# Optimization experiments

Measured on AMD Instinct MI355X. Metric: run time of the kernel, lower is better.

## Reference

```python
import jax, jax.numpy as jnp
import numpy as np

N_HEAD, D_MODEL, D_K, D_V = 8, 512, 64, 64
B, S = 4, 2048
LN_EPS = 1e-5


def setup_inputs() -> dict:
    key = jax.random.key(0)
    ks = jax.random.split(key, 12)
    std_qk = np.sqrt(2.0 / (D_MODEL + D_K))
    std_v = np.sqrt(2.0 / (D_MODEL + D_V))
    return {
        "q": jax.random.normal(ks[0], (B, S, D_MODEL), jnp.float32),
        "k": jax.random.normal(ks[1], (B, S, D_MODEL), jnp.float32),
        "v": jax.random.normal(ks[2], (B, S, D_MODEL), jnp.float32),
        "w_qs": jax.random.normal(ks[3], (N_HEAD * D_K, D_MODEL), jnp.float32) * std_qk,
        "b_qs": jnp.zeros((N_HEAD * D_K,), jnp.float32),
        "w_ks": jax.random.normal(ks[4], (N_HEAD * D_K, D_MODEL), jnp.float32) * std_qk,
        "b_ks": jnp.zeros((N_HEAD * D_K,), jnp.float32),
        "w_vs": jax.random.normal(ks[5], (N_HEAD * D_V, D_MODEL), jnp.float32) * std_v,
        "b_vs": jnp.zeros((N_HEAD * D_V,), jnp.float32),
        "w_fc": jax.random.normal(ks[6], (D_MODEL, N_HEAD * D_V), jnp.float32) * np.sqrt(2.0 / (D_MODEL + N_HEAD * D_V)),
        "b_fc": jnp.zeros((D_MODEL,), jnp.float32),
        "ln_g": jnp.ones((D_MODEL,), jnp.float32),
        "ln_b": jnp.zeros((D_MODEL,), jnp.float32),
    }


def reference(q, k, v, w_qs, b_qs, w_ks, b_ks, w_vs, b_vs, w_fc, b_fc, ln_g, ln_b):
    sz_b, len_q, _ = q.shape
    residual = q
    temperature = np.power(D_K, 0.5).astype(np.float32)
    # Projections: [b, s, h*dk] -> [h, b, s, dk]  (matches permute(2,0,1,3))
    qh = (jnp.einsum('bsd,fd->bsf', q, w_qs) + b_qs).reshape(sz_b, len_q, N_HEAD, D_K).transpose(2, 0, 1, 3)
    kh = (jnp.einsum('bsd,fd->bsf', k, w_ks) + b_ks).reshape(sz_b, -1, N_HEAD, D_K).transpose(2, 0, 1, 3)
    vh = (jnp.einsum('bsd,fd->bsf', v, w_vs) + b_vs).reshape(sz_b, -1, N_HEAD, D_V).transpose(2, 0, 1, 3)
    # Scaled dot-product attention (dropout is identity in eval)
    attn = jnp.einsum('hbqd,hbkd->hbqk', qh, kh) / temperature
    attn = jax.nn.softmax(attn, axis=-1)
    out = jnp.einsum('hbqk,hbkv->hbqv', attn, vh)          # [h, b, q, dv]
    out = out.transpose(1, 2, 0, 3).reshape(sz_b, len_q, N_HEAD * D_V)
    out = jnp.einsum('bsf,df->bsd', out, w_fc) + b_fc
    # Residual + LayerNorm
    x = out + residual
    mu = jnp.mean(x, axis=-1, keepdims=True)
    var = jnp.mean(jnp.square(x - mu), axis=-1, keepdims=True)
    x = (x - mu) * jax.lax.rsqrt(var + LN_EPS) * ln_g + ln_b
    # attn returned as [(n_head*b), len_q, len_k] to match torch bmm layout
    return x, attn.reshape(N_HEAD * sz_b, len_q, -1)
```

## Files before the change

kernel.cpp:

```cpp
#include <hip/hip_runtime.h>
#include <hip/hip_bf16.h>

constexpr int NB  = 4;
constexpr int NS  = 2048;
constexpr int NH  = 8;
constexpr int DM  = 512;
constexpr int DKV = 64;
constexpr int HB  = NH * NB;

typedef __attribute__((ext_vector_type(8))) short short8;
typedef __attribute__((ext_vector_type(4))) float f32x4;

__device__ inline unsigned short f2bf(float f) {
    unsigned u = __builtin_bit_cast(unsigned, f);
    u = (u + 0x7fffu + ((u >> 16) & 1u)) >> 16;
    return (unsigned short)u;
}
__device__ inline float bf2f(unsigned short h) {
    unsigned u = ((unsigned)h) << 16;
    return __builtin_bit_cast(float, u);
}
__device__ inline short8 ld8(const unsigned short* p) { return *(const short8*)p; }

__device__ inline short8 pack8(const float* p) {
    f32x4 a = *(const f32x4*)p;
    f32x4 b = *(const f32x4*)(p + 4);
    short8 r;
    r[0] = (short)f2bf(a[0]); r[1] = (short)f2bf(a[1]);
    r[2] = (short)f2bf(a[2]); r[3] = (short)f2bf(a[3]);
    r[4] = (short)f2bf(b[0]); r[5] = (short)f2bf(b[1]);
    r[6] = (short)f2bf(b[2]); r[7] = (short)f2bf(b[3]);
    return r;
}

__device__ inline f32x4 mfma16(short8 a, short8 b, f32x4 c) {
    return __builtin_amdgcn_mfma_f32_16x16x32_bf16(a, b, c, 0, 0, 0);
}

__device__ inline void gl_lds16(const void* g, void* l) {
    __builtin_amdgcn_global_load_lds(
        (const __attribute__((address_space(1))) unsigned*)g,
        (__attribute__((address_space(3))) unsigned*)l, 16, 0, 0);
}

__device__ inline void bar() { __builtin_amdgcn_s_barrier(); }

__global__ __launch_bounds__(256) void k_cvtw(const float* __restrict__ s0,
                                              const float* __restrict__ s1,
                                              const float* __restrict__ s2,
                                              const float* __restrict__ s3,
                                              unsigned short* __restrict__ d0,
                                              unsigned short* __restrict__ d1,
                                              unsigned short* __restrict__ d2,
                                              unsigned short* __restrict__ d3)
{
    const float* s; unsigned short* d;
    switch (blockIdx.y) {
        case 0:  s = s0; d = d0; break;
        case 1:  s = s1; d = d1; break;
        case 2:  s = s2; d = d2; break;
        default: s = s3; d = d3; break;
    }
    const size_t i = ((size_t)blockIdx.x * 256 + threadIdx.x) * 8;
    *(short8*)(d + i) = pack8(s + i);
}

__global__ __launch_bounds__(256, 4) void k_proj3(const float* __restrict__ Xq,
                                                  const float* __restrict__ Xk,
                                                  const float* __restrict__ Xv,
                                                  const unsigned short* __restrict__ Wq,
                                                  const unsigned short* __restrict__ Wk,
                                                  const unsigned short* __restrict__ Wv,
                                                  const float* __restrict__ bq,
                                                  const float* __restrict__ bk,
                                                  const float* __restrict__ bv,
                                                  unsigned short* __restrict__ oq,
                                                  unsigned short* __restrict__ ok,
                                                  unsigned short* __restrict__ ov)
{
    const float* X; const unsigned short* W; const float* bias; unsigned short* out;
    float scale = 1.0f; int vtrans = 0;
    switch (blockIdx.z) {
        case 0:  X = Xq; W = Wq; bias = bq; out = oq;
                 scale = 0.125f * 1.44269504088896340736f; break;
        case 1:  X = Xk; W = Wk; bias = bk; out = ok; break;
        default: X = Xv; W = Wv; bias = bv; out = ov; vtrans = 1; break;
    }
    const int tid = threadIdx.x;
    const int l = tid & 63, w = tid >> 6;
    const int c = l & 15, g = l >> 4;
    const int m0 = blockIdx.y * 64 + w * 16;
    const int f0 = blockIdx.x * 64;
    const int arow = m0 + c;

    f32x4 acc[4] = {};
    const float* aB = X + (size_t)arow * DM;
    for (int kb = 0; kb < DM; kb += 32) {
        short8 af = pack8(aB + kb + g * 8);
#pragma unroll
        for (int n = 0; n < 4; ++n) {
            short8 bf = ld8(W + (size_t)(f0 + n * 16 + c) * DM + kb + g * 8);
            acc[n] = mfma16(af, bf, acc[n]);
        }
    }
#pragma unroll
    for (int n = 0; n < 4; ++n) {
        const int f = f0 + n * 16 + c;
        const int h = f >> 6, d = f & 63;
        const float bvv = bias[f];
#pragma unroll
        for (int r = 0; r < 4; ++r) {
            const int m = m0 + g * 4 + r;
            const int bb = m >> 11, s = m & (NS - 1);
            const int hb = h * NB + bb;
            const float v = (acc[n][r] + bvv) * scale;
            const size_t idx = vtrans ? ((size_t)(hb * DKV + d) * NS + s)
                                      : ((size_t)(hb * NS + s) * DKV + d);
            out[idx] = f2bf(v);
        }
    }
}

__global__ __launch_bounds__(256, 4) void k_attn(const unsigned short* __restrict__ Qh,
                                                 const unsigned short* __restrict__ Kh,
                                                 const unsigned short* __restrict__ Vt,
                                                 float* __restrict__ attn,
                                                 unsigned short* __restrict__ Obuf)
{
    __shared__ __align__(16) char kld[2][8192];
    __shared__ __align__(16) char vld[2][8192];
    __shared__ __align__(16) char plds[4 * 2048];
    const int tid = threadIdx.x;
    const int l = tid & 63, w = tid >> 6;
    const int c = l & 15, g = l >> 4;
    constexpr int NT = NS / 64;

    const int bid = blockIdx.x;
    const int wid = (bid & 7) * 128 + (bid >> 3);
    const int hb = wid >> 5;
    const int q0 = (wid & 31) * 64 + w * 16;
    char* myp = plds + w * 2048;

    const char* kbytes = (const char*)(Kh + (size_t)hb * NS * DKV);
    const char* vbytes = (const char*)(Vt + (size_t)hb * DKV * NS);

    const unsigned short* qb = Qh + ((size_t)hb * NS + q0 + c) * DKV + g * 8;
    const short8 qf0 = ld8(qb), qf1 = ld8(qb + 32);

    int koff[2], voff[2];
#pragma unroll
    for (int j = 0; j < 2; ++j) {
        const int D = (w * 2 + j) * 1024 + l * 16;
        const int row = D >> 7;
        const int scolb = (D & 127) ^ ((row & 7) << 4);
        koff[j] = row * 128 + scolb;
        voff[j] = row * (NS * 2) + scolb;
    }
    const int swc = (c & 7) << 4;

    const int ldsbase = w * 2048;

    float ls[4] = {0.f, 0.f, 0.f, 0.f};
    {
        gl_lds16(kbytes + koff[0], kld[0] + ldsbase);
        gl_lds16(kbytes + koff[1], kld[0] + ldsbase + 1024);
        asm volatile("s_waitcnt vmcnt(0)" ::: "memory");
        bar();
        __builtin_amdgcn_sched_barrier(0);
        int cur = 0;
        for (int kt = 0; kt < NT; ++kt) {
            if (kt + 1 < NT) {
                const size_t nb = (size_t)(kt + 1) * 64 * 128;
                gl_lds16(kbytes + nb + koff[0], kld[cur ^ 1] + ldsbase);
                gl_lds16(kbytes + nb + koff[1], kld[cur ^ 1] + ldsbase + 1024);
            }
            if (kt > 0) {
                if (kt + 1 < NT) { asm volatile("s_waitcnt vmcnt(2)" ::: "memory"); }
                else             { asm volatile("s_waitcnt vmcnt(0)" ::: "memory"); }
                bar();
                __builtin_amdgcn_sched_barrier(0);
            }
#pragma unroll
            for (int t = 0; t < 4; ++t) {
                const int rb = (t * 16 + c) * 128;
                const short8 b0 = *(const short8*)(kld[cur] + rb + ((g * 16) ^ swc));
                const short8 b1 = *(const short8*)(kld[cur] + rb + ((64 + g * 16) ^ swc));
                f32x4 z = {};
                z = mfma16(qf0, b0, z);
                z = mfma16(qf1, b1, z);
#pragma unroll
                for (int r = 0; r < 4; ++r) ls[r] += exp2f(z[r]);
            }
            bar();
            cur ^= 1;
        }
    }
    float li[4];
#pragma unroll
    for (int r = 0; r < 4; ++r) {
        float s = ls[r];
        s += __shfl_xor(s, 1);
        s += __shfl_xor(s, 2);
        s += __shfl_xor(s, 4);
        s += __shfl_xor(s, 8);
        li[r] = 1.0f / s;
    }

    f32x4 oacc[4] = {};
    float* abase = attn + (size_t)hb * NS * NS + (size_t)(q0 + g * 4) * NS + c;

    {
        gl_lds16(kbytes + koff[0], kld[0] + ldsbase);
        gl_lds16(kbytes + koff[1], kld[0] + ldsbase + 1024);
        gl_lds16(vbytes + voff[0], vld[0] + ldsbase);
        gl_lds16(vbytes + voff[1], vld[0] + ldsbase + 1024);
        asm volatile("s_waitcnt vmcnt(0)" ::: "memory");
        bar();
        __builtin_amdgcn_sched_barrier(0);
        int cur = 0;
        for (int kt = 0; kt < NT; ++kt) {
            const int k0 = kt * 64;
            if (kt + 1 < NT) {
                const size_t nkb = (size_t)(k0 + 64) * 128;
                const size_t nvb = (size_t)(k0 + 64) * 2;
                gl_lds16(kbytes + nkb + koff[0], kld[cur ^ 1] + ldsbase);
                gl_lds16(kbytes + nkb + koff[1], kld[cur ^ 1] + ldsbase + 1024);
                gl_lds16(vbytes + nvb + voff[0], vld[cur ^ 1] + ldsbase);
                gl_lds16(vbytes + nvb + voff[1], vld[cur ^ 1] + ldsbase + 1024);
            }
            if (kt > 0) {
                if (kt + 1 < NT) { asm volatile("s_waitcnt vmcnt(20)" ::: "memory"); }
                else             { asm volatile("s_waitcnt vmcnt(16)" ::: "memory"); }
                bar();
                __builtin_amdgcn_sched_barrier(0);
            }
            f32x4 sc[4];
#pragma unroll
            for (int t = 0; t < 4; ++t) {
                const int rb = (t * 16 + c) * 128;
                const short8 b0 = *(const short8*)(kld[cur] + rb + ((g * 16) ^ swc));
                const short8 b1 = *(const short8*)(kld[cur] + rb + ((64 + g * 16) ^ swc));
                f32x4 z = {};
                z = mfma16(qf0, b0, z);
                z = mfma16(qf1, b1, z);
                sc[t] = z;
            }
#pragma unroll
            for (int t = 0; t < 4; ++t)
#pragma unroll
                for (int r = 0; r < 4; ++r) {
                    const float p = exp2f(sc[t][r]) * li[r];
                    abase[(size_t)r * NS + k0 + t * 16] = p;
                    const int row = g * 4 + r;
                    int by = row * 128 + (t * 16 + c) * 2;
                    by ^= (row & 7) << 4;
                    *(unsigned short*)(myp + by) = f2bf(p);
                }
            asm volatile("s_waitcnt lgkmcnt(0)" ::: "memory");
            __builtin_amdgcn_sched_barrier(0);
#pragma unroll
            for (int kk = 0; kk < 2; ++kk) {
                const short8 pa = *(const short8*)(myp + c * 128 + ((kk * 64 + g * 16) ^ swc));
#pragma unroll
                for (int n = 0; n < 4; ++n) {
                    const int rb = (n * 16 + c) * 128;
                    const short8 vb = *(const short8*)(vld[cur] + rb + ((kk * 64 + g * 16) ^ swc));
                    oacc[n] = mfma16(pa, vb, oacc[n]);
                }
            }
            bar();
            cur ^= 1;
        }
    }

    const int h = hb >> 2, bb = hb & 3;
#pragma unroll
    for (int n = 0; n < 4; ++n)
#pragma unroll
        for (int r = 0; r < 4; ++r) {
            const int q = q0 + g * 4 + r;
            const int dv = n * 16 + c;
            Obuf[((size_t)(bb * NS + q)) * DM + h * DKV + dv] = f2bf(oacc[n][r]);
        }
}

__global__ __launch_bounds__(256, 4) void k_fc(const unsigned short* __restrict__ O,
                                            const unsigned short* __restrict__ Wfc,
                                            const float* __restrict__ bfc,
                                            const float* __restrict__ resid,
                                            unsigned short* __restrict__ Y)
{
    const int tid = threadIdx.x;
    const int l = tid & 63, w = tid >> 6;
    const int c = l & 15, g = l >> 4;
    const int m0 = blockIdx.y * 64 + w * 16;
    const int f0 = blockIdx.x * 64;
    const int arow = m0 + c;

    f32x4 acc[4] = {};
    const unsigned short* aB = O + (size_t)arow * DM;
    for (int kb = 0; kb < DM; kb += 32) {
        short8 af = ld8(aB + kb + g * 8);
#pragma unroll
        for (int n = 0; n < 4; ++n) {
            short8 bf = ld8(Wfc + (size_t)(f0 + n * 16 + c) * DM + kb + g * 8);
            acc[n] = mfma16(af, bf, acc[n]);
        }
    }
#pragma unroll
    for (int n = 0; n < 4; ++n) {
        const int d = f0 + n * 16 + c;
        const float bv = bfc[d];
#pragma unroll
        for (int r = 0; r < 4; ++r) {
            const int m = m0 + g * 4 + r;
            const float v = acc[n][r] + bv + resid[(size_t)m * DM + d];
            Y[(size_t)m * DM + d] = f2bf(v);
        }
    }
}

__global__ __launch_bounds__(256) void k_ln(const unsigned short* __restrict__ Y,
                                            const float* __restrict__ gam,
                                            const float* __restrict__ bet,
                                            float* __restrict__ out)
{
    const int tid = threadIdx.x;
    const int l = tid & 63, w = tid >> 6;
    const int row = blockIdx.x * 4 + w;

    const short8 yv = ld8(Y + (size_t)row * DM + l * 8);
    float x[8];
#pragma unroll
    for (int j = 0; j < 8; ++j) x[j] = bf2f((unsigned short)yv[j]);

    float s = 0.f;
#pragma unroll
    for (int j = 0; j < 8; ++j) s += x[j];
#pragma unroll
    for (int mask = 1; mask <= 32; mask <<= 1) s += __shfl_xor(s, mask);
    const float mean = s * (1.0f / DM);

    float d2 = 0.f;
#pragma unroll
    for (int j = 0; j < 8; ++j) { const float t = x[j] - mean; d2 += t * t; }
#pragma unroll
    for (int mask = 1; mask <= 32; mask <<= 1) d2 += __shfl_xor(d2, mask);
    const float rstd = rsqrtf(d2 * (1.0f / DM) + 1e-5f);

#pragma unroll
    for (int j = 0; j < 8; ++j) {
        const int d = l * 8 + j;
        out[(size_t)row * DM + d] = (x[j] - mean) * rstd * gam[d] + bet[d];
    }
}

extern "C" void kernel_launch(void* const* d_in, const int* in_sizes, int n_in,
                              void* d_out, int out_size, void* d_ws, size_t ws_size,
                              hipStream_t stream)
{
    const float* q    = (const float*)d_in[0];
    const float* k    = (const float*)d_in[1];
    const float* v    = (const float*)d_in[2];
    const float* w_qs = (const float*)d_in[3];
    const float* b_qs = (const float*)d_in[4];
    const float* w_ks = (const float*)d_in[5];
    const float* b_ks = (const float*)d_in[6];
    const float* w_vs = (const float*)d_in[7];
    const float* b_vs = (const float*)d_in[8];
    const float* w_fc = (const float*)d_in[9];
    const float* b_fc = (const float*)d_in[10];
    const float* ln_g = (const float*)d_in[11];
    const float* ln_b = (const float*)d_in[12];

    char* ws = (char*)d_ws;
    unsigned short* Qh = (unsigned short*)(ws);
    unsigned short* Kh = (unsigned short*)(ws + (8u  << 20));
    unsigned short* Vt = (unsigned short*)(ws + (16u << 20));
    unsigned short* Ob = (unsigned short*)(ws + (24u << 20));
    unsigned short* Yb = (unsigned short*)(ws + (32u << 20));
    unsigned short* Wq = (unsigned short*)(ws + (40u << 20));
    unsigned short* Wk = Wq + (size_t)DM * DM;
    unsigned short* Wv = Wk + (size_t)DM * DM;
    unsigned short* Wf = Wv + (size_t)DM * DM;

    float* xout = (float*)d_out;
    float* attn = xout + (size_t)NB * NS * DM;

    k_cvtw<<<dim3(128, 4), 256, 0, stream>>>(w_qs, w_ks, w_vs, w_fc, Wq, Wk, Wv, Wf);

    k_proj3<<<dim3(8, 128, 3), 256, 0, stream>>>(q, k, v, Wq, Wk, Wv,
                                                 b_qs, b_ks, b_vs, Qh, Kh, Vt);

    k_attn<<<1024, 256, 0, stream>>>(Qh, Kh, Vt, attn, Ob);

    k_fc<<<dim3(8, 128), 256, 0, stream>>>(Ob, Wf, b_fc, q, Yb);
    k_ln<<<NB * NS / 4, 256, 0, stream>>>(Yb, ln_g, ln_b, xout);
}
```

Measured before the change: 399.8 us.

## Process 32 query rows per wave in attention to double K/V tile reuse

Each wave in the attention kernel now handles two 16-row query subtiles (128 queries per block instead of 64), so every K and V tile loaded into LDS feeds twice as many MFMAs. The grid is halved, launch bounds drop to 2 blocks per SM, the P staging buffer doubles, and the vmcnt wait thresholds are raised to account for the doubled attn global stores. This cuts K/V global-to-LDS traffic and barrier overhead per unit of work. In exchange it raises register pressure and lowers occupancy. The kernel is likely bound by the large fp32 attn writes anyway.

```diff
diff --git a/kernel.cpp b/kernel.cpp
--- a/kernel.cpp
+++ b/kernel.cpp
@@ -121,7 +121,7 @@
     }
 }
 
-__global__ __launch_bounds__(256, 4) void k_attn(const unsigned short* __restrict__ Qh,
+__global__ __launch_bounds__(256, 2) void k_attn(const unsigned short* __restrict__ Qh,
                                                  const unsigned short* __restrict__ Kh,
                                                  const unsigned short* __restrict__ Vt,
                                                  float* __restrict__ attn,
@@ -129,23 +129,27 @@
 {
     __shared__ __align__(16) char kld[2][8192];
     __shared__ __align__(16) char vld[2][8192];
-    __shared__ __align__(16) char plds[4 * 2048];
+    __shared__ __align__(16) char plds[4 * 4096];
     const int tid = threadIdx.x;
     const int l = tid & 63, w = tid >> 6;
     const int c = l & 15, g = l >> 4;
     constexpr int NT = NS / 64;
 
     const int bid = blockIdx.x;
-    const int wid = (bid & 7) * 128 + (bid >> 3);
-    const int hb = wid >> 5;
-    const int q0 = (wid & 31) * 64 + w * 16;
-    char* myp = plds + w * 2048;
+    const int wid = (bid & 7) * 64 + (bid >> 3);
+    const int hb = wid >> 4;
+    const int q0 = (wid & 15) * 128 + w * 32;
+    char* myp = plds + w * 4096;
 
     const char* kbytes = (const char*)(Kh + (size_t)hb * NS * DKV);
     const char* vbytes = (const char*)(Vt + (size_t)hb * DKV * NS);
 
-    const unsigned short* qb = Qh + ((size_t)hb * NS + q0 + c) * DKV + g * 8;
-    const short8 qf0 = ld8(qb), qf1 = ld8(qb + 32);
+    short8 qf[2][2];
+#pragma unroll
+    for (int s2 = 0; s2 < 2; ++s2) {
+        const unsigned short* qb = Qh + ((size_t)hb * NS + q0 + s2 * 16 + c) * DKV + g * 8;
+        qf[s2][0] = ld8(qb); qf[s2][1] = ld8(qb + 32);
+    }
 
     int koff[2], voff[2];
 #pragma unroll
@@ -160,7 +164,7 @@
 
     const int ldsbase = w * 2048;
 
-    float ls[4] = {0.f, 0.f, 0.f, 0.f};
+    float ls[2][4] = {};
     {
         gl_lds16(kbytes + koff[0], kld[0] + ldsbase);
         gl_lds16(kbytes + koff[1], kld[0] + ldsbase + 1024);
@@ -185,28 +189,33 @@
                 const int rb = (t * 16 + c) * 128;
                 const short8 b0 = *(const short8*)(kld[cur] + rb + ((g * 16) ^ swc));
                 const short8 b1 = *(const short8*)(kld[cur] + rb + ((64 + g * 16) ^ swc));
-                f32x4 z = {};
-                z = mfma16(qf0, b0, z);
-                z = mfma16(qf1, b1, z);
-#pragma unroll
-                for (int r = 0; r < 4; ++r) ls[r] += exp2f(z[r]);
+#pragma unroll
+                for (int s2 = 0; s2 < 2; ++s2) {
+                    f32x4 z = {};
+                    z = mfma16(qf[s2][0], b0, z);
+                    z = mfma16(qf[s2][1], b1, z);
+#pragma unroll
+                    for (int r = 0; r < 4; ++r) ls[s2][r] += exp2f(z[r]);
+                }
             }
             bar();
             cur ^= 1;
         }
     }
-    float li[4];
-#pragma unroll
-    for (int r = 0; r < 4; ++r) {
-        float s = ls[r];
-        s += __shfl_xor(s, 1);
-        s += __shfl_xor(s, 2);
-        s += __shfl_xor(s, 4);
-        s += __shfl_xor(s, 8);
-        li[r] = 1.0f / s;
-    }
-
-    f32x4 oacc[4] = {};
+    float li[2][4];
+#pragma unroll
+    for (int s2 = 0; s2 < 2; ++s2)
+#pragma unroll
+        for (int r = 0; r < 4; ++r) {
+            float s = ls[s2][r];
+            s += __shfl_xor(s, 1);
+            s += __shfl_xor(s, 2);
+            s += __shfl_xor(s, 4);
+            s += __shfl_xor(s, 8);
+            li[s2][r] = 1.0f / s;
+        }
+
+    f32x4 oacc[2][4] = {};
     float* abase = attn + (size_t)hb * NS * NS + (size_t)(q0 + g * 4) * NS + c;
 
     {
@@ -229,43 +238,50 @@
                 gl_lds16(vbytes + nvb + voff[1], vld[cur ^ 1] + ldsbase + 1024);
             }
             if (kt > 0) {
-                if (kt + 1 < NT) { asm volatile("s_waitcnt vmcnt(20)" ::: "memory"); }
-                else             { asm volatile("s_waitcnt vmcnt(16)" ::: "memory"); }
+                if (kt + 1 < NT) { asm volatile("s_waitcnt vmcnt(36)" ::: "memory"); }
+                else             { asm volatile("s_waitcnt vmcnt(32)" ::: "memory"); }
                 bar();
                 __builtin_amdgcn_sched_barrier(0);
             }
-            f32x4 sc[4];
+            f32x4 sc[2][4];
 #pragma unroll
             for (int t = 0; t < 4; ++t) {
                 const int rb = (t * 16 + c) * 128;
                 const short8 b0 = *(const short8*)(kld[cur] + rb + ((g * 16) ^ swc));
                 const short8 b1 = *(const short8*)(kld[cur] + rb + ((64 + g * 16) ^ swc));
-                f32x4 z = {};
-                z = mfma16(qf0, b0, z);
-                z = mfma16(qf1, b1, z);
-                sc[t] = z;
-            }
-#pragma unroll
-            for (int t = 0; t < 4; ++t)
-#pragma unroll
-                for (int r = 0; r < 4; ++r) {
-                    const float p = exp2f(sc[t][r]) * li[r];
-                    abase[(size_t)r * NS + k0 + t * 16] = p;
-                    const int row = g * 4 + r;
-                    int by = row * 128 + (t * 16 + c) * 2;
-                    by ^= (row & 7) << 4;
-                    *(unsigned short*)(myp + by) = f2bf(p);
+#pragma unroll
+                for (int s2 = 0; s2 < 2; ++s2) {
+                    f32x4 z = {};
+                    z = mfma16(qf[s2][0], b0, z);
+                    z = mfma16(qf[s2][1], b1, z);
+                    sc[s2][t] = z;
                 }
+            }
+#pragma unroll
+            for (int s2 = 0; s2 < 2; ++s2)
+#pragma unroll
+                for (int t = 0; t < 4; ++t)
+#pragma unroll
+                    for (int r = 0; r < 4; ++r) {
+                        const float p = exp2f(sc[s2][t][r]) * li[s2][r];
+                        abase[(size_t)(s2 * 16 + r) * NS + k0 + t * 16] = p;
+                        const int row = s2 * 16 + g * 4 + r;
+                        int by = row * 128 + (t * 16 + c) * 2;
+                        by ^= (row & 7) << 4;
+                        *(unsigned short*)(myp + by) = f2bf(p);
+                    }
             asm volatile("s_waitcnt lgkmcnt(0)" ::: "memory");
             __builtin_amdgcn_sched_barrier(0);
 #pragma unroll
             for (int kk = 0; kk < 2; ++kk) {
-                const short8 pa = *(const short8*)(myp + c * 128 + ((kk * 64 + g * 16) ^ swc));
+                const short8 pa0 = *(const short8*)(myp + c * 128 + ((kk * 64 + g * 16) ^ swc));
+                const short8 pa1 = *(const short8*)(myp + (16 + c) * 128 + ((kk * 64 + g * 16) ^ swc));
 #pragma unroll
                 for (int n = 0; n < 4; ++n) {
                     const int rb = (n * 16 + c) * 128;
                     const short8 vb = *(const short8*)(vld[cur] + rb + ((kk * 64 + g * 16) ^ swc));
-                    oacc[n] = mfma16(pa, vb, oacc[n]);
+                    oacc[0][n] = mfma16(pa0, vb, oacc[0][n]);
+                    oacc[1][n] = mfma16(pa1, vb, oacc[1][n]);
                 }
             }
             bar();
@@ -275,13 +291,15 @@
 
     const int h = hb >> 2, bb = hb & 3;
 #pragma unroll
-    for (int n = 0; n < 4; ++n)
-#pragma unroll
-        for (int r = 0; r < 4; ++r) {
-            const int q = q0 + g * 4 + r;
-            const int dv = n * 16 + c;
-            Obuf[((size_t)(bb * NS + q)) * DM + h * DKV + dv] = f2bf(oacc[n][r]);
-        }
+    for (int s2 = 0; s2 < 2; ++s2)
+#pragma unroll
+        for (int n = 0; n < 4; ++n)
+#pragma unroll
+            for (int r = 0; r < 4; ++r) {
+                const int q = q0 + s2 * 16 + g * 4 + r;
+                const int dv = n * 16 + c;
+                Obuf[((size_t)(bb * NS + q)) * DM + h * DKV + dv] = f2bf(oacc[s2][n][r]);
+            }
 }
 
 __global__ __launch_bounds__(256, 4) void k_fc(const unsigned short* __restrict__ O,
@@ -392,7 +410,7 @@
     k_proj3<<<dim3(8, 128, 3), 256, 0, stream>>>(q, k, v, Wq, Wk, Wv,
                                                  b_qs, b_ks, b_vs, Qh, Kh, Vt);
 
-    k_attn<<<1024, 256, 0, stream>>>(Qh, Kh, Vt, attn, Ob);
+    k_attn<<<512, 256, 0, stream>>>(Qh, Kh, Vt, attn, Ob);
 
     k_fc<<<dim3(8, 128), 256, 0, stream>>>(Ob, Wf, b_fc, q, Yb);
     k_ln<<<NB * NS / 4, 256, 0, stream>>>(Yb, ln_g, ln_b, xout);
```

Result: no change. 402.4 us (+0.7%).
